# Performance work log

Measured on AMD Instinct MI355X. Metric: run time of the kernel, lower is better.

The kernel has to match this reference:

```python
import jax, jax.numpy as jnp
import numpy as np
import math

B, T, E, D = 4, 2048, 1024, 4

def _tau_init(t):
    a = 0.1 ** (1.0 / max(t - 1, 1))
    tt = -math.log(max(a, 1e-10))
    return math.log(math.exp(tt) - 1 + 1e-10)

def causal_ema(b, tau_raw):
    # h_t = alpha * h_{t-1} + b_t with alpha = exp(-softplus(tau_raw));
    # exactly equal to the conv1d with kernel exp(-tau*j) in the original.
    alpha = jnp.exp(-jax.nn.softplus(tau_raw)).astype(b.dtype)
    def step(h, bt):
        h = alpha * h + bt
        return h, h
    h0 = jnp.zeros((b.shape[0], b.shape[2]), b.dtype)
    _, hs = jax.lax.scan(step, h0, jnp.swapaxes(b, 0, 1))  # scan over T
    return jnp.swapaxes(hs, 0, 1)

def setup_inputs():
    key = jax.random.key(0)
    ks = jax.random.split(key, 10)
    s = 0.02
    return {
        "x": jax.random.normal(ks[0], (B, T, E), jnp.float32),
        "tau_ctx": jnp.float32(_tau_init(max(T // 2, 4))),
        "tau_raws": jnp.array([_tau_init(max(T // 2 ** i, 2)) for i in range(D)], jnp.float32),
        "Wg": jax.random.normal(ks[1], (E, 2 * E), jnp.float32) * s,
        "bg": jnp.full((E,), -0.5, jnp.float32),
        "Wn1": jax.random.normal(ks[2], (E // 4, E), jnp.float32) * s,
        "bn1": jnp.zeros((E // 4,), jnp.float32),
        "Wn2": jax.random.normal(ks[3], (D, E // 4), jnp.float32) * s,
        "bn2": jnp.zeros((D,), jnp.float32),
        "blend": jax.random.normal(ks[4], (D, E), jnp.float32) * s,
        "Wsoma": jax.random.normal(ks[5], (E, E), jnp.float32) * s,
        "bsoma": jnp.zeros((E,), jnp.float32),
        "Wtemp": jax.random.normal(ks[6], (E, E), jnp.float32) * s,
        "btemp": jnp.zeros((E,), jnp.float32),
        "Wout": jax.random.normal(ks[7], (E, E), jnp.float32) * s,
        "gamma": jnp.ones((E,), jnp.float32),
        "beta": jnp.zeros((E,), jnp.float32),
    }

def reference(x, tau_ctx, tau_raws, Wg, bg, Wn1, bn1, Wn2, bn2, blend, Wsoma, bsoma, Wtemp, btemp, Wout, gamma, beta):
    ctx = causal_ema(x, tau_ctx)                                   # (B,T,E)
    gate_in = jnp.concatenate([x, ctx], axis=-1)                   # (B,T,2E)
    wg = jax.nn.sigmoid(jnp.einsum('btc,ec->bte', gate_in, Wg) + bg)
    gated = x * wg
    h1 = jax.nn.gelu(jnp.einsum('btc,hc->bth', x, Wn1) + bn1, approximate=False)
    mod = 0.5 + jax.nn.sigmoid(jnp.einsum('bth,dh->btd', h1, Wn2) + bn2)  # (B,T,D)
    # neuromod_ema: modulate input then fixed-alpha EMA, one per dendrite
    traces = jax.vmap(lambda tau, m: causal_ema(gated * m[..., None], tau))(
        tau_raws, jnp.moveaxis(mod, -1, 0))                        # (D,B,T,E)
    blend_w = jax.nn.softmax(blend, axis=0)                        # (D,E)
    temporal = jnp.einsum('dbtc,dc->btc', traces, blend_w)
    gate = jax.nn.sigmoid(jnp.einsum('btc,ec->bte', temporal, Wtemp) + btemp)
    soma = jax.nn.gelu(jnp.einsum('btc,ec->bte', x, Wsoma) + bsoma, approximate=False)
    out = jnp.einsum('btc,ec->bte', soma * gate, Wout)
    mu = out.mean(-1, keepdims=True)
    var = out.var(-1, keepdims=True)
    return (out - mu) / jnp.sqrt(var + 1e-5) * gamma + beta
```

## Files before the change

### kernel.cpp

```cpp
#include <hip/hip_runtime.h>
#include <math.h>

#define B_DIM 4
#define T_DIM 2048
#define E_DIM 1024
#define M_ROWS (B_DIM*T_DIM)
#define NC 32
#define CL (T_DIM/NC)

typedef short short8 __attribute__((ext_vector_type(8)));
typedef float f32x4 __attribute__((ext_vector_type(4)));

__device__ __forceinline__ float bf2f(unsigned short u){
  union { unsigned int i; float f; } c; c.i = ((unsigned int)u) << 16; return c.f;
}
__device__ __forceinline__ unsigned short f2bf(float f){
  union { float f; unsigned int i; } c; c.f = f;
  unsigned int u = c.i;
  return (unsigned short)((u + 0x7FFFu + ((u >> 16) & 1u)) >> 16);
}
__device__ __forceinline__ unsigned int pack2(float a, float b){
  return (unsigned int)f2bf(a) | ((unsigned int)f2bf(b) << 16);
}
__device__ __forceinline__ float sigf(float x){ return 1.f/(1.f+__expf(-x)); }
__device__ __forceinline__ float geluf(float x){ return 0.5f*x*(1.f+erff(x*0.70710678118f)); }

__device__ __forceinline__ void glds16(const unsigned short* g, unsigned short* l){
  __builtin_amdgcn_global_load_lds((const __attribute__((address_space(1))) void*)g,
                                   (__attribute__((address_space(3))) void*)l, 16, 0, 0);
}

__device__ __forceinline__ void cvt4(const float* __restrict__ s, unsigned short* __restrict__ d){
  float4 v = *(const float4*)s;
  uint2 p; p.x = pack2(v.x, v.y); p.y = pack2(v.z, v.w);
  *(uint2*)d = p;
}

__global__ __launch_bounds__(256) void conv_carry_k(
    const float* __restrict__ Wg, const float* __restrict__ Wsoma,
    const float* __restrict__ Wn1, const float* __restrict__ Wtemp,
    const float* __restrict__ Wout, const float* __restrict__ bsoma,
    const float* __restrict__ bn1,
    unsigned short* __restrict__ wg_bf, unsigned short* __restrict__ wsn1,
    unsigned short* __restrict__ wtemp_bf, unsigned short* __restrict__ wout_bf,
    float* __restrict__ bsn1,
    const float* __restrict__ x, const float* __restrict__ tau_ctx,
    float* __restrict__ car){
  if (blockIdx.x < 5378){
    int u = blockIdx.x*256 + threadIdx.x;
    if (u < 524288){ cvt4(Wg + (size_t)u*4, wg_bf + (size_t)u*4); }
    else if (u < 786432){ u -= 524288; cvt4(Wsoma + (size_t)u*4, wsn1 + (size_t)u*4); }
    else if (u < 851968){ u -= 786432; cvt4(Wn1 + (size_t)u*4, wsn1 + 1048576 + (size_t)u*4); }
    else if (u < 1114112){ u -= 851968; cvt4(Wtemp + (size_t)u*4, wtemp_bf + (size_t)u*4); }
    else if (u < 1376256){ u -= 1114112; cvt4(Wout + (size_t)u*4, wout_bf + (size_t)u*4); }
    else if (u < 1376576){
      u -= 1376256; int i = u*4;
      float4 v = (i < 1024) ? *(const float4*)&bsoma[i] : *(const float4*)&bn1[i-1024];
      *(float4*)&bsn1[i] = v;
    }
  } else {
    int gid = (blockIdx.x - 5378)*256 + threadIdx.x;
    int e2 = (gid & 511)*2, bc = gid >> 9;
    int b = bc >> 5, chunk = bc & 31;
    float alpha = 1.f/(1.f+expf(tau_ctx[0]));
    const float2* xp = (const float2*)(x + ((size_t)b*T_DIM + chunk*CL)*E_DIM + e2);
    float h0 = 0.f, h1 = 0.f;
    #pragma unroll 8
    for (int t = 0; t < CL; t++){
      float2 v = xp[(size_t)t*512];
      h0 = alpha*h0 + v.x; h1 = alpha*h1 + v.y;
    }
    *(float2*)&car[(size_t)bc*E_DIM + e2] = make_float2(h0, h1);
  }
}

__global__ __launch_bounds__(256) void ctx_scan_k(const float* __restrict__ x,
                                                  const float* __restrict__ tau_ctx,
                                                  const float* __restrict__ car,
                                                  unsigned short* __restrict__ gatein){
  int gid = blockIdx.x*256 + threadIdx.x;
  int e2 = (gid & 511)*2, bc = gid >> 9;
  int b = bc >> 5, chunk = bc & 31;
  float alpha = 1.f/(1.f+expf(tau_ctx[0]));
  float alphaL = powf(alpha, (float)CL);
  float h0 = 0.f, h1 = 0.f;
  for (int j = 0; j < chunk; j++){
    float2 c = *(const float2*)&car[(size_t)(b*NC + j)*E_DIM + e2];
    h0 = alphaL*h0 + c.x; h1 = alphaL*h1 + c.y;
  }
  const float2* xp = (const float2*)(x + ((size_t)b*T_DIM + chunk*CL)*E_DIM + e2);
  unsigned int* op = (unsigned int*)(gatein + ((size_t)(b*T_DIM + chunk*CL))*2048 + e2);
  #pragma unroll 4
  for (int t = 0; t < CL; t++){
    float2 v = xp[(size_t)t*512];
    h0 = alpha*h0 + v.x; h1 = alpha*h1 + v.y;
    op[(size_t)t*1024]       = pack2(v.x, v.y);
    op[(size_t)t*1024 + 512] = pack2(h0, h1);
  }
}

__global__ __launch_bounds__(256) void dend_carry_k(const unsigned short* __restrict__ gated,
                                                    const float* __restrict__ mod,
                                                    const float* __restrict__ tau_raws,
                                                    float* __restrict__ car){
  int gid = blockIdx.x*256 + threadIdx.x;
  int e2 = (gid & 511)*2, bc = gid >> 9;
  int b = bc >> 5, chunk = bc & 31;
  float a[4];
  #pragma unroll
  for (int d = 0; d < 4; d++) a[d] = 1.f/(1.f+expf(tau_raws[d]));
  const ushort2* gp = (const ushort2*)(gated + ((size_t)(b*T_DIM + chunk*CL))*E_DIM + e2);
  const float4* mp = (const float4*)(mod + (size_t)(b*T_DIM + chunk*CL)*4);
  float hx[4] = {0,0,0,0}, hy[4] = {0,0,0,0};
  #pragma unroll 4
  for (int t = 0; t < CL; t++){
    ushort2 gv = gp[(size_t)t*512];
    float gx = bf2f(gv.x), gy = bf2f(gv.y);
    float4 m4 = mp[t];
    hx[0] = a[0]*hx[0] + gx*m4.x; hy[0] = a[0]*hy[0] + gy*m4.x;
    hx[1] = a[1]*hx[1] + gx*m4.y; hy[1] = a[1]*hy[1] + gy*m4.y;
    hx[2] = a[2]*hx[2] + gx*m4.z; hy[2] = a[2]*hy[2] + gy*m4.z;
    hx[3] = a[3]*hx[3] + gx*m4.w; hy[3] = a[3]*hy[3] + gy*m4.w;
  }
  #pragma unroll
  for (int d = 0; d < 4; d++)
    *(float2*)&car[(size_t)d*131072 + (size_t)bc*E_DIM + e2] = make_float2(hx[d], hy[d]);
}

__global__ __launch_bounds__(256) void dend_scan_k(const unsigned short* __restrict__ gated,
                                                   const float* __restrict__ mod,
                                                   const float* __restrict__ tau_raws,
                                                   const float* __restrict__ car,
                                                   const float* __restrict__ blend,
                                                   unsigned short* __restrict__ temporal){
  int gid = blockIdx.x*256 + threadIdx.x;
  int e2 = (gid & 511)*2, bc = gid >> 9;
  int b = bc >> 5, chunk = bc & 31;
  float a[4], hx[4], hy[4];
  #pragma unroll
  for (int d = 0; d < 4; d++) a[d] = 1.f/(1.f+expf(tau_raws[d]));
  #pragma unroll
  for (int d = 0; d < 4; d++){
    float aL = powf(a[d], (float)CL);
    float h0 = 0.f, h1 = 0.f;
    for (int j = 0; j < chunk; j++){
      float2 c = *(const float2*)&car[(size_t)d*131072 + (size_t)(b*NC + j)*E_DIM + e2];
      h0 = aL*h0 + c.x; h1 = aL*h1 + c.y;
    }
    hx[d] = h0; hy[d] = h1;
  }
  float blx[4], bly[4];
  #pragma unroll
  for (int d = 0; d < 4; d++){
    float2 bl = *(const float2*)&blend[(size_t)d*E_DIM + e2];
    blx[d] = bl.x; bly[d] = bl.y;
  }
  float mxx = fmaxf(fmaxf(blx[0],blx[1]), fmaxf(blx[2],blx[3]));
  float mxy = fmaxf(fmaxf(bly[0],bly[1]), fmaxf(bly[2],bly[3]));
  float wx[4], wy[4], sx = 0.f, sy = 0.f;
  #pragma unroll
  for (int d = 0; d < 4; d++){ wx[d] = __expf(blx[d]-mxx); sx += wx[d];
                               wy[d] = __expf(bly[d]-mxy); sy += wy[d]; }
  float ix = 1.f/sx, iy = 1.f/sy;
  #pragma unroll
  for (int d = 0; d < 4; d++){ wx[d] *= ix; wy[d] *= iy; }

  const ushort2* gp = (const ushort2*)(gated + ((size_t)(b*T_DIM + chunk*CL))*E_DIM + e2);
  const float4* mp = (const float4*)(mod + (size_t)(b*T_DIM + chunk*CL)*4);
  unsigned int* op = (unsigned int*)(temporal + ((size_t)(b*T_DIM + chunk*CL))*E_DIM + e2);
  #pragma unroll 4
  for (int t = 0; t < CL; t++){
    ushort2 gv = gp[(size_t)t*512];
    float gx = bf2f(gv.x), gy = bf2f(gv.y);
    float4 m4 = mp[t];
    hx[0] = a[0]*hx[0] + gx*m4.x; hy[0] = a[0]*hy[0] + gy*m4.x;
    hx[1] = a[1]*hx[1] + gx*m4.y; hy[1] = a[1]*hy[1] + gy*m4.y;
    hx[2] = a[2]*hx[2] + gx*m4.z; hy[2] = a[2]*hy[2] + gy*m4.z;
    hx[3] = a[3]*hx[3] + gx*m4.w; hy[3] = a[3]*hy[3] + gy*m4.w;
    float tvx = wx[0]*hx[0] + wx[1]*hx[1] + wx[2]*hx[2] + wx[3]*hx[3];
    float tvy = wy[0]*hy[0] + wy[1]*hy[1] + wy[2]*hy[2] + wy[3]*hy[3];
    op[(size_t)t*512] = pack2(tvx, tvy);
  }
}

__global__ __launch_bounds__(256) void mod_k(const unsigned short* __restrict__ h1,
                                             const float* __restrict__ Wn2,
                                             const float* __restrict__ bn2,
                                             float* __restrict__ mod){
  int wave = threadIdx.x >> 6, lane = threadIdx.x & 63;
  int m = blockIdx.x*4 + wave;
  float p0=0.f,p1=0.f,p2=0.f,p3=0.f;
  for (int c = lane; c < 256; c += 64){
    float h = bf2f(h1[(size_t)m*256 + c]);
    p0 += h*Wn2[0*256 + c]; p1 += h*Wn2[1*256 + c];
    p2 += h*Wn2[2*256 + c]; p3 += h*Wn2[3*256 + c];
  }
  #pragma unroll
  for (int off = 32; off > 0; off >>= 1){
    p0 += __shfl_down(p0, off); p1 += __shfl_down(p1, off);
    p2 += __shfl_down(p2, off); p3 += __shfl_down(p3, off);
  }
  if (lane == 0){
    mod[(size_t)m*4 + 0] = 0.5f + sigf(p0 + bn2[0]);
    mod[(size_t)m*4 + 1] = 0.5f + sigf(p1 + bn2[1]);
    mod[(size_t)m*4 + 2] = 0.5f + sigf(p2 + bn2[2]);
    mod[(size_t)m*4 + 3] = 0.5f + sigf(p3 + bn2[3]);
  }
}

__global__ __launch_bounds__(256, 2) void gemm1_k(
    const unsigned short* __restrict__ gatein,
    const unsigned short* __restrict__ wg_bf,
    const unsigned short* __restrict__ wsn1,
    const float* __restrict__ bg,
    const float* __restrict__ bsn1,
    unsigned short* __restrict__ gated,
    unsigned short* __restrict__ soma,
    unsigned short* __restrict__ h1)
{
  __shared__ unsigned short sA[2][4096];
  __shared__ unsigned short sB[2][4096];
  const int tid = threadIdx.x;
  const int wv = tid >> 6, lane = tid & 63;
  const int quad = lane >> 4, l15 = lane & 15;
  const int wm = (wv & 1) * 64, wn = (wv >> 1) * 64;
  const int row0 = blockIdx.x * 128;
  const int by = blockIdx.y;

  int mode, colw0, K;
  const unsigned short* Bw;
  const float* bias;
  if (by < 8)       { mode = 0; colw0 = by*128;             Bw = wg_bf + (size_t)colw0*2048; K = 2048; bias = bg   + colw0; }
  else if (by < 16) { mode = 1; colw0 = (by-8)*128;         Bw = wsn1  + (size_t)colw0*1024; K = 1024; bias = bsn1 + colw0; }
  else              { mode = 2; colw0 = 1024 + (by-16)*128; Bw = wsn1  + (size_t)colw0*1024; K = 1024; bias = bsn1 + colw0; }

  const int rr = lane >> 2;
  const int qs = (lane & 3) ^ ((rr >> 1) & 3);
  const int kc = qs * 8;
  const unsigned short* pa0 = gatein + (size_t)(row0 + wv*16 + rr)*2048 + kc;
  const unsigned short* pa1 = pa0 + (size_t)64*2048;
  const unsigned short* pb0 = Bw + (size_t)(wv*16 + rr)*K + kc;
  const unsigned short* pb1 = pb0 + (size_t)64*K;

  f32x4 acc[4][4];
  #pragma unroll
  for (int i = 0; i < 4; i++)
    #pragma unroll
    for (int j = 0; j < 4; j++) acc[i][j] = (f32x4){0.f,0.f,0.f,0.f};

  glds16(pa0, &sA[0][wv*512]);
  glds16(pa1, &sA[0][2048 + wv*512]);
  glds16(pb0, &sB[0][wv*512]);
  glds16(pb1, &sB[0][2048 + wv*512]);

  const int swr = (l15 >> 1) & 3;
  const int nk = K >> 5;
  for (int it = 0; it < nk; it++){
    __syncthreads();
    const int cur = it & 1, nxt = cur ^ 1;
    if (it + 1 < nk){
      const int ko = (it + 1) << 5;
      glds16(pa0 + ko, &sA[nxt][wv*512]);
      glds16(pa1 + ko, &sA[nxt][2048 + wv*512]);
      glds16(pb0 + ko, &sB[nxt][wv*512]);
      glds16(pb1 + ko, &sB[nxt][2048 + wv*512]);
    }
    short8 afr[4], bfr[4];
    #pragma unroll
    for (int i = 0; i < 4; i++) afr[i] = *(const short8*)&sA[cur][(wm + i*16 + l15)*32 + (quad ^ swr)*8];
    #pragma unroll
    for (int j = 0; j < 4; j++) bfr[j] = *(const short8*)&sB[cur][(wn + j*16 + l15)*32 + (quad ^ swr)*8];
    #pragma unroll
    for (int i = 0; i < 4; i++)
      #pragma unroll
      for (int j = 0; j < 4; j++)
        acc[i][j] = __builtin_amdgcn_mfma_f32_16x16x32_bf16(afr[i], bfr[j], acc[i][j], 0, 0, 0);
  }

  if (mode == 0){
    #pragma unroll
    for (int i = 0; i < 4; i++)
      #pragma unroll
      for (int j = 0; j < 4; j++){
        const int lc = wn + j*16 + l15;
        const int col = colw0 + lc;
        #pragma unroll
        for (int rr2 = 0; rr2 < 4; rr2++){
          const int row = row0 + wm + i*16 + quad*4 + rr2;
          float v = acc[i][j][rr2] + bias[lc];
          float xv = bf2f(gatein[(size_t)row*2048 + col]);
          gated[(size_t)row*1024 + col] = f2bf(xv * sigf(v));
        }
      }
  } else if (mode == 1){
    #pragma unroll
    for (int i = 0; i < 4; i++)
      #pragma unroll
      for (int j = 0; j < 4; j++){
        const int lc = wn + j*16 + l15;
        const int col = colw0 + lc;
        #pragma unroll
        for (int rr2 = 0; rr2 < 4; rr2++){
          const int row = row0 + wm + i*16 + quad*4 + rr2;
          float v = acc[i][j][rr2] + bias[lc];
          soma[(size_t)row*1024 + col] = f2bf(geluf(v));
        }
      }
  } else {
    #pragma unroll
    for (int i = 0; i < 4; i++)
      #pragma unroll
      for (int j = 0; j < 4; j++){
        const int lc = wn + j*16 + l15;
        const int col = colw0 - 1024 + lc;
        #pragma unroll
        for (int rr2 = 0; rr2 < 4; rr2++){
          const int row = row0 + wm + i*16 + quad*4 + rr2;
          float v = acc[i][j][rr2] + bias[lc];
          h1[(size_t)row*256 + col] = f2bf(geluf(v));
        }
      }
  }
}

template<int EPI>
__global__ __launch_bounds__(256, 2) void gemm_k(
    const unsigned short* __restrict__ A,
    const unsigned short* __restrict__ Bw,
    const float* __restrict__ bias,
    const unsigned short* __restrict__ ebf,
    void* __restrict__ outp)
{
  __shared__ unsigned short sA[2][4096];
  __shared__ unsigned short sB[2][4096];
  const int tid = threadIdx.x;
  const int wv = tid >> 6, lane = tid & 63;
  const int quad = lane >> 4, l15 = lane & 15;
  const int wm = (wv & 1) * 64, wn = (wv >> 1) * 64;
  const int row0 = blockIdx.x * 128, col0 = blockIdx.y * 128;

  const int rr = lane >> 2;
  const int qs = (lane & 3) ^ ((rr >> 1) & 3);
  const int kc = qs * 8;
  const unsigned short* pa0 = A  + (size_t)(row0 + wv*16 + rr)*1024 + kc;
  const unsigned short* pa1 = pa0 + (size_t)64*1024;
  const unsigned short* pb0 = Bw + (size_t)(col0 + wv*16 + rr)*1024 + kc;
  const unsigned short* pb1 = pb0 + (size_t)64*1024;

  f32x4 acc[4][4];
  #pragma unroll
  for (int i = 0; i < 4; i++)
    #pragma unroll
    for (int j = 0; j < 4; j++) acc[i][j] = (f32x4){0.f,0.f,0.f,0.f};

  glds16(pa0, &sA[0][wv*512]);
  glds16(pa1, &sA[0][2048 + wv*512]);
  glds16(pb0, &sB[0][wv*512]);
  glds16(pb1, &sB[0][2048 + wv*512]);

  const int swr = (l15 >> 1) & 3;
  for (int it = 0; it < 32; it++){
    __syncthreads();
    const int cur = it & 1, nxt = cur ^ 1;
    if (it + 1 < 32){
      const int ko = (it + 1) << 5;
      glds16(pa0 + ko, &sA[nxt][wv*512]);
      glds16(pa1 + ko, &sA[nxt][2048 + wv*512]);
      glds16(pb0 + ko, &sB[nxt][wv*512]);
      glds16(pb1 + ko, &sB[nxt][2048 + wv*512]);
    }
    short8 afr[4], bfr[4];
    #pragma unroll
    for (int i = 0; i < 4; i++) afr[i] = *(const short8*)&sA[cur][(wm + i*16 + l15)*32 + (quad ^ swr)*8];
    #pragma unroll
    for (int j = 0; j < 4; j++) bfr[j] = *(const short8*)&sB[cur][(wn + j*16 + l15)*32 + (quad ^ swr)*8];
    #pragma unroll
    for (int i = 0; i < 4; i++)
      #pragma unroll
      for (int j = 0; j < 4; j++)
        acc[i][j] = __builtin_amdgcn_mfma_f32_16x16x32_bf16(afr[i], bfr[j], acc[i][j], 0, 0, 0);
  }

  #pragma unroll
  for (int i = 0; i < 4; i++)
    #pragma unroll
    for (int j = 0; j < 4; j++){
      const int col = col0 + wn + j*16 + l15;
      #pragma unroll
      for (int rr2 = 0; rr2 < 4; rr2++){
        const int row = row0 + wm + i*16 + quad*4 + rr2;
        float v = acc[i][j][rr2];
        size_t o = (size_t)row*1024 + col;
        if (EPI == 2){
          v += bias[col];
          ((unsigned short*)outp)[o] = f2bf(sigf(v) * bf2f(ebf[o]));
        } else {
          ((float*)outp)[o] = v;
        }
      }
    }
}

__global__ __launch_bounds__(256) void ln_k(const float* __restrict__ in,
                                            const float* __restrict__ gamma,
                                            const float* __restrict__ beta,
                                            float* __restrict__ out){
  int wv = threadIdx.x >> 6, lane = threadIdx.x & 63;
  int row = blockIdx.x*4 + wv;
  const float4* ip = (const float4*)&in[(size_t)row*1024];
  float4 v[4];
  float s = 0.f, q = 0.f;
  #pragma unroll
  for (int k = 0; k < 4; k++){
    v[k] = ip[lane + 64*k];
    s += v[k].x + v[k].y + v[k].z + v[k].w;
    q += v[k].x*v[k].x + v[k].y*v[k].y + v[k].z*v[k].z + v[k].w*v[k].w;
  }
  #pragma unroll
  for (int off = 32; off > 0; off >>= 1){
    s += __shfl_xor(s, off); q += __shfl_xor(q, off);
  }
  float mu = s*(1.f/1024.f);
  float var = q*(1.f/1024.f) - mu*mu;
  float rs = rsqrtf(var + 1e-5f);
  const float4* gp = (const float4*)gamma;
  const float4* bp = (const float4*)beta;
  float4* op = (float4*)&out[(size_t)row*1024];
  #pragma unroll
  for (int k = 0; k < 4; k++){
    int idx = lane + 64*k;
    float4 g = gp[idx], bb = bp[idx];
    float4 o;
    o.x = (v[k].x-mu)*rs*g.x + bb.x;
    o.y = (v[k].y-mu)*rs*g.y + bb.y;
    o.z = (v[k].z-mu)*rs*g.z + bb.z;
    o.w = (v[k].w-mu)*rs*g.w + bb.w;
    op[idx] = o;
  }
}

extern "C" void kernel_launch(void* const* d_in, const int* in_sizes, int n_in,
                              void* d_out, int out_size, void* d_ws, size_t ws_size,
                              hipStream_t stream) {
  const float* x        = (const float*)d_in[0];
  const float* tau_ctx  = (const float*)d_in[1];
  const float* tau_raws = (const float*)d_in[2];
  const float* Wg       = (const float*)d_in[3];
  const float* bg       = (const float*)d_in[4];
  const float* Wn1      = (const float*)d_in[5];
  const float* bn1      = (const float*)d_in[6];
  const float* Wn2      = (const float*)d_in[7];
  const float* bn2      = (const float*)d_in[8];
  const float* blend    = (const float*)d_in[9];
  const float* Wsoma    = (const float*)d_in[10];
  const float* bsoma    = (const float*)d_in[11];
  const float* Wtemp    = (const float*)d_in[12];
  const float* btemp    = (const float*)d_in[13];
  const float* Wout     = (const float*)d_in[14];
  const float* gamma    = (const float*)d_in[15];
  const float* beta     = (const float*)d_in[16];

  char* ws = (char*)d_ws;
  unsigned short* gatein   = (unsigned short*)(ws + 0);
  float*          out_pre  = (float*)(ws + 0);
  unsigned short* wg_bf    = (unsigned short*)(ws + 33554432);
  unsigned short* wsn1     = (unsigned short*)(ws + 37748736);
  unsigned short* wtemp_bf = (unsigned short*)(ws + 40370176);
  unsigned short* wout_bf  = (unsigned short*)(ws + 42467328);
  float*          bsn1     = (float*)(ws + 44564480);
  unsigned short* h1_bf    = (unsigned short*)(ws + 44572672);
  float*          car_d    = (float*)(ws + 44572672);
  float*          car_ctx  = (float*)(ws + 48766976);
  float*          modbuf   = (float*)(ws + 48766976);
  unsigned short* gated    = (unsigned short*)(ws + 49291264);
  unsigned short* sg       = gated;
  unsigned short* temporal = (unsigned short*)(ws + 66068480);
  unsigned short* soma     = (unsigned short*)(ws + 82845696);

  conv_carry_k<<<dim3(5634), dim3(256), 0, stream>>>(Wg, Wsoma, Wn1, Wtemp, Wout, bsoma, bn1,
                                                     wg_bf, wsn1, wtemp_bf, wout_bf, bsn1,
                                                     x, tau_ctx, car_ctx);

  ctx_scan_k<<<dim3(256), dim3(256), 0, stream>>>(x, tau_ctx, car_ctx, gatein);

  gemm1_k<<<dim3(64, 18), dim3(256), 0, stream>>>(gatein, wg_bf, wsn1, bg, bsn1,
                                                  gated, soma, h1_bf);

  mod_k<<<dim3(M_ROWS/4), dim3(256), 0, stream>>>(h1_bf, Wn2, bn2, modbuf);

  dend_carry_k<<<dim3(256), dim3(256), 0, stream>>>(gated, modbuf, tau_raws, car_d);
  dend_scan_k <<<dim3(256), dim3(256), 0, stream>>>(gated, modbuf, tau_raws, car_d, blend, temporal);

  gemm_k<2><<<dim3(64, 8), dim3(256), 0, stream>>>(temporal, wtemp_bf, btemp, soma, sg);

  gemm_k<3><<<dim3(64, 8), dim3(256), 0, stream>>>(sg, wout_bf, nullptr, nullptr, out_pre);

  ln_k<<<dim3(M_ROWS/4), dim3(256), 0, stream>>>(out_pre, gamma, beta, (float*)d_out);
}
```

Measured before the change: 357.2 us.

## Double scan chunk count and add separate carry-prefix kernels

Raises the number of time chunks per sequence from 32 to 64, which doubles the thread count of the carry and scan kernels for better GPU occupancy. The serial carry accumulation that each scan thread previously redid over all earlier chunks is moved into small dedicated prefix kernels that write per-chunk start states. This removes the redundant O(chunk) carry loops but adds two extra launches and serial prefix kernels with very few blocks. Workspace buffers are relocated to hold the larger carry and start arrays.

```diff
diff --git a/kernel.cpp b/kernel.cpp
--- a/kernel.cpp
+++ b/kernel.cpp
@@ -5,7 +5,7 @@
 #define T_DIM 2048
 #define E_DIM 1024
 #define M_ROWS (B_DIM*T_DIM)
-#define NC 32
+#define NC 64
 #define CL (T_DIM/NC)
 
 typedef short short8 __attribute__((ext_vector_type(8)));
@@ -61,7 +61,7 @@
   } else {
     int gid = (blockIdx.x - 5378)*256 + threadIdx.x;
     int e2 = (gid & 511)*2, bc = gid >> 9;
-    int b = bc >> 5, chunk = bc & 31;
+    int b = bc >> 6, chunk = bc & 63;
     float alpha = 1.f/(1.f+expf(tau_ctx[0]));
     const float2* xp = (const float2*)(x + ((size_t)b*T_DIM + chunk*CL)*E_DIM + e2);
     float h0 = 0.f, h1 = 0.f;
@@ -74,20 +74,32 @@
   }
 }
 
+__global__ __launch_bounds__(256) void ctx_prefix_k(const float* __restrict__ car,
+                                                    const float* __restrict__ tau_ctx,
+                                                    float* __restrict__ start){
+  int gid = blockIdx.x*256 + threadIdx.x;
+  int e2 = (gid & 511)*2, b = gid >> 9;
+  float alpha = 1.f/(1.f+expf(tau_ctx[0]));
+  float aL = powf(alpha, (float)CL);
+  float h0 = 0.f, h1 = 0.f;
+  for (int j = 0; j < NC; j++){
+    size_t idx = (size_t)(b*NC + j)*E_DIM + e2;
+    *(float2*)&start[idx] = make_float2(h0, h1);
+    float2 c = *(const float2*)&car[idx];
+    h0 = aL*h0 + c.x; h1 = aL*h1 + c.y;
+  }
+}
+
 __global__ __launch_bounds__(256) void ctx_scan_k(const float* __restrict__ x,
                                                   const float* __restrict__ tau_ctx,
-                                                  const float* __restrict__ car,
+                                                  const float* __restrict__ start,
                                                   unsigned short* __restrict__ gatein){
   int gid = blockIdx.x*256 + threadIdx.x;
   int e2 = (gid & 511)*2, bc = gid >> 9;
-  int b = bc >> 5, chunk = bc & 31;
+  int b = bc >> 6, chunk = bc & 63;
   float alpha = 1.f/(1.f+expf(tau_ctx[0]));
-  float alphaL = powf(alpha, (float)CL);
-  float h0 = 0.f, h1 = 0.f;
-  for (int j = 0; j < chunk; j++){
-    float2 c = *(const float2*)&car[(size_t)(b*NC + j)*E_DIM + e2];
-    h0 = alphaL*h0 + c.x; h1 = alphaL*h1 + c.y;
-  }
+  float2 st = *(const float2*)&start[(size_t)bc*E_DIM + e2];
+  float h0 = st.x, h1 = st.y;
   const float2* xp = (const float2*)(x + ((size_t)b*T_DIM + chunk*CL)*E_DIM + e2);
   unsigned int* op = (unsigned int*)(gatein + ((size_t)(b*T_DIM + chunk*CL))*2048 + e2);
   #pragma unroll 4
@@ -99,13 +111,15 @@
   }
 }
 
+#define DSTRIDE (B_DIM*NC*E_DIM)
+
 __global__ __launch_bounds__(256) void dend_carry_k(const unsigned short* __restrict__ gated,
                                                     const float* __restrict__ mod,
                                                     const float* __restrict__ tau_raws,
                                                     float* __restrict__ car){
   int gid = blockIdx.x*256 + threadIdx.x;
   int e2 = (gid & 511)*2, bc = gid >> 9;
-  int b = bc >> 5, chunk = bc & 31;
+  int b = bc >> 6, chunk = bc & 63;
   float a[4];
   #pragma unroll
   for (int d = 0; d < 4; d++) a[d] = 1.f/(1.f+expf(tau_raws[d]));
@@ -124,30 +138,42 @@
   }
   #pragma unroll
   for (int d = 0; d < 4; d++)
-    *(float2*)&car[(size_t)d*131072 + (size_t)bc*E_DIM + e2] = make_float2(hx[d], hy[d]);
+    *(float2*)&car[(size_t)d*DSTRIDE + (size_t)bc*E_DIM + e2] = make_float2(hx[d], hy[d]);
+}
+
+__global__ __launch_bounds__(256) void dend_prefix_k(const float* __restrict__ car,
+                                                     const float* __restrict__ tau_raws,
+                                                     float* __restrict__ start){
+  int gid = blockIdx.x*256 + threadIdx.x;
+  int e = gid & 1023;
+  int bd = gid >> 10;
+  int b = bd & 3, d = bd >> 2;
+  float alpha = 1.f/(1.f+expf(tau_raws[d]));
+  float aL = powf(alpha, (float)CL);
+  float h = 0.f;
+  const float* cp = car + (size_t)d*DSTRIDE + (size_t)b*NC*E_DIM + e;
+  float* sp = start + (size_t)d*DSTRIDE + (size_t)b*NC*E_DIM + e;
+  for (int j = 0; j < NC; j++){
+    sp[(size_t)j*E_DIM] = h;
+    h = aL*h + cp[(size_t)j*E_DIM];
+  }
 }
 
 __global__ __launch_bounds__(256) void dend_scan_k(const unsigned short* __restrict__ gated,
                                                    const float* __restrict__ mod,
                                                    const float* __restrict__ tau_raws,
-                                                   const float* __restrict__ car,
+                                                   const float* __restrict__ start,
                                                    const float* __restrict__ blend,
                                                    unsigned short* __restrict__ temporal){
   int gid = blockIdx.x*256 + threadIdx.x;
   int e2 = (gid & 511)*2, bc = gid >> 9;
-  int b = bc >> 5, chunk = bc & 31;
+  int b = bc >> 6, chunk = bc & 63;
   float a[4], hx[4], hy[4];
   #pragma unroll
-  for (int d = 0; d < 4; d++) a[d] = 1.f/(1.f+expf(tau_raws[d]));
-  #pragma unroll
   for (int d = 0; d < 4; d++){
-    float aL = powf(a[d], (float)CL);
-    float h0 = 0.f, h1 = 0.f;
-    for (int j = 0; j < chunk; j++){
-      float2 c = *(const float2*)&car[(size_t)d*131072 + (size_t)(b*NC + j)*E_DIM + e2];
-      h0 = aL*h0 + c.x; h1 = aL*h1 + c.y;
-    }
-    hx[d] = h0; hy[d] = h1;
+    a[d] = 1.f/(1.f+expf(tau_raws[d]));
+    float2 st = *(const float2*)&start[(size_t)d*DSTRIDE + (size_t)bc*E_DIM + e2];
+    hx[d] = st.x; hy[d] = st.y;
   }
   float blx[4], bly[4];
   #pragma unroll
@@ -462,6 +488,8 @@
 
   char* ws = (char*)d_ws;
   unsigned short* gatein   = (unsigned short*)(ws + 0);
+  float*          car_d    = (float*)(ws + 0);
+  float*          start_d  = (float*)(ws + 4194304);
   float*          out_pre  = (float*)(ws + 0);
   unsigned short* wg_bf    = (unsigned short*)(ws + 33554432);
   unsigned short* wsn1     = (unsigned short*)(ws + 37748736);
@@ -469,27 +497,30 @@
   unsigned short* wout_bf  = (unsigned short*)(ws + 42467328);
   float*          bsn1     = (float*)(ws + 44564480);
   unsigned short* h1_bf    = (unsigned short*)(ws + 44572672);
-  float*          car_d    = (float*)(ws + 44572672);
-  float*          car_ctx  = (float*)(ws + 48766976);
+  float*          car_ctx  = (float*)(ws + 44572672);
+  float*          start_ctx= (float*)(ws + 45621248);
   float*          modbuf   = (float*)(ws + 48766976);
-  unsigned short* gated    = (unsigned short*)(ws + 49291264);
+  unsigned short* gated    = (unsigned short*)(ws + 48898048);
   unsigned short* sg       = gated;
-  unsigned short* temporal = (unsigned short*)(ws + 66068480);
-  unsigned short* soma     = (unsigned short*)(ws + 82845696);
-
-  conv_carry_k<<<dim3(5634), dim3(256), 0, stream>>>(Wg, Wsoma, Wn1, Wtemp, Wout, bsoma, bn1,
+  unsigned short* temporal = (unsigned short*)(ws + 65675264);
+  unsigned short* soma     = (unsigned short*)(ws + 82452480);
+
+  conv_carry_k<<<dim3(5890), dim3(256), 0, stream>>>(Wg, Wsoma, Wn1, Wtemp, Wout, bsoma, bn1,
                                                      wg_bf, wsn1, wtemp_bf, wout_bf, bsn1,
                                                      x, tau_ctx, car_ctx);
 
-  ctx_scan_k<<<dim3(256), dim3(256), 0, stream>>>(x, tau_ctx, car_ctx, gatein);
+  ctx_prefix_k<<<dim3(8), dim3(256), 0, stream>>>(car_ctx, tau_ctx, start_ctx);
+
+  ctx_scan_k<<<dim3(512), dim3(256), 0, stream>>>(x, tau_ctx, start_ctx, gatein);
 
   gemm1_k<<<dim3(64, 18), dim3(256), 0, stream>>>(gatein, wg_bf, wsn1, bg, bsn1,
                                                   gated, soma, h1_bf);
 
   mod_k<<<dim3(M_ROWS/4), dim3(256), 0, stream>>>(h1_bf, Wn2, bn2, modbuf);
 
-  dend_carry_k<<<dim3(256), dim3(256), 0, stream>>>(gated, modbuf, tau_raws, car_d);
-  dend_scan_k <<<dim3(256), dim3(256), 0, stream>>>(gated, modbuf, tau_raws, car_d, blend, temporal);
+  dend_carry_k<<<dim3(512), dim3(256), 0, stream>>>(gated, modbuf, tau_raws, car_d);
+  dend_prefix_k<<<dim3(64), dim3(256), 0, stream>>>(car_d, tau_raws, start_d);
+  dend_scan_k <<<dim3(512), dim3(256), 0, stream>>>(gated, modbuf, tau_raws, start_d, blend, temporal);
 
   gemm_k<2><<<dim3(64, 8), dim3(256), 0, stream>>>(temporal, wtemp_bf, btemp, soma, sg);
 
```

Result: faster. 324.2 us (-9.2%).
